# Optimization experiments

Measured on AMD Instinct MI355X. Metric: run time of the kernel, lower is better.

## Reference

```python
import jax, jax.numpy as jnp
import numpy as np

HEAD_SIZE = 64


def q_shift_multihead(x, ph, pw, head_dim=HEAD_SIZE, shift=1):
    # x: [B, T, C], T == ph*pw. Quarter-wise spatial shifts per head channel block.
    B, T, C = x.shape
    a = jnp.transpose(x, (0, 2, 1)).reshape(B, C // head_dim, head_dim, ph, pw)
    q = head_dim // 4
    out = jnp.zeros_like(a)
    out = out.at[:, :, 0:q, :, shift:].set(a[:, :, 0:q, :, :-shift])          # shift right in W
    out = out.at[:, :, q:2 * q, :, :-shift].set(a[:, :, q:2 * q, :, shift:])  # shift left in W
    out = out.at[:, :, 2 * q:3 * q, shift:, :].set(a[:, :, 2 * q:3 * q, :-shift, :])  # shift down in H
    out = out.at[:, :, 3 * q:, :-shift, :].set(a[:, :, 3 * q:, shift:, :])            # shift up in H
    return jnp.transpose(out.reshape(B, C, T), (0, 2, 1))


def wkv6(r, k, v, w, u):
    # RWKV-6 linear recurrence. r,k,v,w: [B,T,C]; u: [H, hs]. Decay applied as exp(-exp(w)).
    B, T, C = r.shape
    H, hs = C // HEAD_SIZE, HEAD_SIZE
    rh = jnp.transpose(r.reshape(B, T, H, hs), (1, 0, 2, 3))
    kh = jnp.transpose(k.reshape(B, T, H, hs), (1, 0, 2, 3))
    vh = jnp.transpose(v.reshape(B, T, H, hs), (1, 0, 2, 3))
    wh = jnp.exp(-jnp.exp(jnp.transpose(w.reshape(B, T, H, hs), (1, 0, 2, 3))))

    def step(S, inp):  # S: [B,H,hs(key j),hs(val i)]
        rt, kt, vt, wt = inp
        kv = kt[..., :, None] * vt[..., None, :]                # [B,H,hs,hs]
        y = jnp.einsum('bhj,bhji->bhi', rt, S + u[None, :, :, None] * kv)
        return wt[..., None] * S + kv, y

    S0 = jnp.zeros((B, H, hs, hs), r.dtype)
    _, ys = jax.lax.scan(step, S0, (rh, kh, vh, wh))
    return jnp.transpose(ys, (1, 0, 2, 3)).reshape(B, T, C)


def group_norm(x, weight, bias, n_groups, eps=1e-5):
    # x: [N, C]
    N, C = x.shape
    g = x.reshape(N, n_groups, C // n_groups)
    mu = g.mean(-1, keepdims=True)
    var = ((g - mu) ** 2).mean(-1, keepdims=True)
    g = (g - mu) / jnp.sqrt(var + eps)
    return g.reshape(N, C) * weight + bias


def setup_inputs() -> dict:
    key = jax.random.key(0)
    B, ph, pw, C = 8, 32, 32, 768
    T = ph * pw
    n_layer, layer_id = 12, 6
    H = C // HEAD_SIZE
    ks = jax.random.split(key, 10)
    x = jax.random.normal(ks[0], (B, T, C), jnp.float32)
    W_r = 0.02 * jax.random.normal(ks[1], (C, C), jnp.float32)
    W_k = 0.02 * jax.random.normal(ks[2], (C, C), jnp.float32)
    W_v = 0.02 * jax.random.normal(ks[3], (C, C), jnp.float32)
    W_g = 0.02 * jax.random.normal(ks[4], (C, C), jnp.float32)
    W_o = 0.02 * jax.random.normal(ks[5], (C, C), jnp.float32)
    r01 = layer_id / (n_layer - 1)
    r10 = 1.0 - layer_id / n_layer
    ddd = np.arange(C, dtype=np.float64) / C
    maa_x = jnp.asarray(1.0 - ddd ** r10, jnp.float32).reshape(1, 1, C)
    maa_w = maa_x
    maa_k = maa_x
    maa_v = jnp.asarray(1.0 - (ddd ** r10 + 0.3 * r01), jnp.float32).reshape(1, 1, C)
    maa_r = jnp.asarray(1.0 - ddd ** (0.5 * r10), jnp.float32).reshape(1, 1, C)
    maa_g = maa_r
    maa_w1 = jax.random.uniform(ks[6], (C, 32 * 5), jnp.float32, -1e-4, 1e-4)
    maa_w2 = jax.random.uniform(ks[7], (5, 32, C), jnp.float32, -1e-4, 1e-4)
    n = np.arange(C, dtype=np.float64)
    time_decay = jnp.asarray(-6 + 5 * (n / (C - 1)) ** (0.7 + 1.3 * r01), jnp.float32).reshape(1, 1, C)
    dec_w1 = jax.random.uniform(ks[8], (C, 64), jnp.float32, -1e-4, 1e-4)
    dec_w2 = jax.random.uniform(ks[9], (64, C), jnp.float32, -1e-4, 1e-4)
    zig = ((n + 1) % 3 - 1) * 0.1
    faaaa = jnp.asarray(r01 * (1 - n / (C - 1)) + zig, jnp.float32).reshape(H, HEAD_SIZE)
    ln_w = jnp.ones((C,), jnp.float32)
    ln_b = jnp.zeros((C,), jnp.float32)
    return dict(x=x, W_r=W_r, W_k=W_k, W_v=W_v, W_g=W_g, W_o=W_o,
                maa_x=maa_x, maa_w=maa_w, maa_k=maa_k, maa_v=maa_v, maa_r=maa_r, maa_g=maa_g,
                maa_w1=maa_w1, maa_w2=maa_w2, time_decay=time_decay,
                dec_w1=dec_w1, dec_w2=dec_w2, faaaa=faaaa, ln_w=ln_w, ln_b=ln_b,
                patch_h=ph, patch_w=pw)


def reference(x, W_r, W_k, W_v, W_g, W_o, maa_x, maa_w, maa_k, maa_v, maa_r, maa_g,
              maa_w1, maa_w2, time_decay, dec_w1, dec_w2, faaaa, ln_w, ln_b,
              patch_h, patch_w):
    B, T, C = x.shape
    xx = q_shift_multihead(x, patch_h, patch_w) - x
    xxx = x + xx * maa_x
    t = jnp.tanh(xxx @ maa_w1).reshape(B, T, 5, 32)
    m = jnp.einsum('btfr,frc->fbtc', t, maa_w2)  # [5,B,T,C]
    mw, mk, mv, mr, mg = m[0], m[1], m[2], m[3], m[4]
    xw = x + xx * (maa_w + mw)
    xk = x + xx * (maa_k + mk)
    xv = x + xx * (maa_v + mv)
    xr = x + xx * (maa_r + mr)
    xg = x + xx * (maa_g + mg)
    r = xr @ W_r.T
    k = xk @ W_k.T
    v = xv @ W_v.T
    g = jax.nn.relu(xg @ W_g.T)
    ww = jnp.tanh(xw @ dec_w1) @ dec_w2
    w = time_decay + ww
    y = wkv6(r, k, v, w, faaaa)
    y = group_norm(y.reshape(B * T, C), ln_w, ln_b, C // HEAD_SIZE).reshape(B, T, C)
    return (y * g) @ W_o.T
```

## Files before the change

### kernel.cpp

```cpp
#include <hip/hip_runtime.h>
#include <math.h>


#define EPI_NONE 0
#define EPI_TANH 1
#define EPI_RELU 2
#define EPI_BIAS 3

typedef float f32x4 __attribute__((ext_vector_type(4)));
typedef __bf16 bf16x8 __attribute__((ext_vector_type(8)));

__device__ __forceinline__ ushort f2bf(float x) {
  unsigned u = __float_as_uint(x);
  return (ushort)((u + 0x7fffu + ((u >> 16) & 1u)) >> 16);
}

#define GLDS16(gp, lp)                                                   \
  __builtin_amdgcn_global_load_lds(                                      \
      (const __attribute__((address_space(1))) void*)(gp),               \
      (__attribute__((address_space(3))) void*)(lp), 16, 0, 0)

__global__ __launch_bounds__(256) void k_qshift(
    const float* __restrict__ x, const float* __restrict__ maa_x,
    ushort* __restrict__ xxx_bf,
    int B, int T, int C, int ph, int pw) {
  long idx = (long)blockIdx.x * blockDim.x + threadIdx.x;
  long total = (long)B * T * C;
  if (idx >= total) return;
  int c = (int)(idx % C);
  long bt = idx / C;
  int t = (int)(bt % T);
  int quarter = (c & 63) >> 4;
  int hh = t / pw;
  int ww = t - hh * pw;
  long rowbase = (bt - t) * C;
  float sval = 0.f;
  int st = -1;
  if (quarter == 0)      { if (ww >= 1)      st = t - 1;  }
  else if (quarter == 1) { if (ww < pw - 1)  st = t + 1;  }
  else if (quarter == 2) { if (hh >= 1)      st = t - pw; }
  else                   { if (hh < ph - 1)  st = t + pw; }
  if (st >= 0) sval = x[rowbase + (long)st * C + c];
  float xval = x[idx];
  float d = sval - xval;
  xxx_bf[idx] = f2bf(xval + d * maa_x[c]);
}

__global__ __launch_bounds__(256) void k_wprep(
    const float* __restrict__ w1, const float* __restrict__ w2,
    const float* __restrict__ dw1, const float* __restrict__ dw2,
    ushort* __restrict__ maa1T, ushort* __restrict__ w2T,
    ushort* __restrict__ w1dT, ushort* __restrict__ w2dT) {
  int idx = blockIdx.x * 256 + threadIdx.x;
  if (idx < 196608) {
    int n = idx / 768, k = idx - n * 768;
    maa1T[idx] = f2bf(n < 160 ? w1[(size_t)k * 160 + n] : 0.f);
  } else if (idx < 196608 + 122880) {
    int j = idx - 196608;
    int c = j / 160, kk = j - c * 160;
    w2T[j] = f2bf(w2[(size_t)kk * 768 + c]);
  } else if (idx < 196608 + 122880 + 98304) {
    int j = idx - (196608 + 122880);
    int n = j / 768, k = j - n * 768;
    w1dT[j] = f2bf(n < 64 ? dw1[(size_t)k * 64 + n] : 0.f);
  } else {
    int j = idx - (196608 + 122880 + 98304);
    int n = j >> 6, k = j & 63;
    w2dT[j] = f2bf(dw2[(size_t)k * 768 + n]);
  }
}

__global__ __launch_bounds__(256) void k_mix5m(
    const ushort* __restrict__ t5b, const ushort* __restrict__ w2T,
    const float* __restrict__ x,
    const float* __restrict__ maa_w, const float* __restrict__ maa_k,
    const float* __restrict__ maa_v, const float* __restrict__ maa_r,
    const float* __restrict__ maa_g,
    ushort* __restrict__ xw, ushort* __restrict__ xk, ushort* __restrict__ xvb,
    ushort* __restrict__ xr, ushort* __restrict__ xg,
    int C, int T, int ph, int pw) {
  int tid = threadIdx.x;
  int lane = tid & 63, wid = tid >> 6;
  int m0 = blockIdx.y * 64, n0 = blockIdx.x * 128;
  int lm = lane & 15, lk = (lane >> 4) * 8;
  int rq = (lane >> 4) * 4;
  const ushort* ap = t5b + (size_t)(m0 + wid * 16 + lm) * 160 + lk;

  int stq[4][4];
#pragma unroll
  for (int q = 0; q < 4; q++) {
    int mr = m0 + wid * 16 + rq + q;
    int t = mr % T;
    int hh = t / pw, ww = t - hh * pw;
    stq[q][0] = (ww >= 1)      ? mr - 1  : -1;
    stq[q][1] = (ww < pw - 1)  ? mr + 1  : -1;
    stq[q][2] = (hh >= 1)      ? mr - pw : -1;
    stq[q][3] = (hh < ph - 1)  ? mr + pw : -1;
  }

  float xh[8][4], dh[8][4];
#pragma unroll
  for (int j = 0; j < 8; j++)
#pragma unroll
    for (int q = 0; q < 4; q++) {
      int mr = m0 + wid * 16 + rq + q;
      int col = n0 + j * 16 + lm;
      float xv = x[(size_t)mr * C + col];
      int sr = stq[q][j & 3];
      float sv = (sr >= 0) ? x[(size_t)sr * C + col] : 0.f;
      xh[j][q] = xv;
      dh[j][q] = sv - xv;
    }

#pragma unroll
  for (int f = 0; f < 5; f++) {
    bf16x8 af = *(const bf16x8*)(ap + f * 32);
    f32x4 acc[8];
#pragma unroll
    for (int j = 0; j < 8; j++) {
      bf16x8 bfj = *(const bf16x8*)(w2T +
          (size_t)(n0 + j * 16 + lm) * 160 + f * 32 + lk);
      acc[j] = __builtin_amdgcn_mfma_f32_16x16x32_bf16(
          af, bfj, (f32x4){0.f, 0.f, 0.f, 0.f}, 0, 0, 0);
    }
    const float* maa_f = (f == 0) ? maa_w : (f == 1) ? maa_k
                        : (f == 2) ? maa_v : (f == 3) ? maa_r : maa_g;
    ushort* dst = (f == 0) ? xw : (f == 1) ? xk
                 : (f == 2) ? xvb : (f == 3) ? xr : xg;
#pragma unroll
    for (int j = 0; j < 8; j++) {
      float mf = maa_f[n0 + j * 16 + lm];
#pragma unroll
      for (int q = 0; q < 4; q++) {
        size_t off = (size_t)(m0 + wid * 16 + rq + q) * C + (n0 + j * 16 + lm);
        dst[off] = f2bf(xh[j][q] + dh[j][q] * (mf + acc[j][q]));
      }
    }
  }
}

__global__ __launch_bounds__(256) void k_cvt5(
    const float* __restrict__ s0, const float* __restrict__ s1,
    const float* __restrict__ s2, const float* __restrict__ s3,
    const float* __restrict__ s4,
    ushort* __restrict__ d0, ushort* __restrict__ d1,
    ushort* __restrict__ d2, ushort* __restrict__ d3,
    ushort* __restrict__ d4, int n) {
  const float* s;
  ushort* d;
  switch (blockIdx.y) {
    case 0: s = s0; d = d0; break;
    case 1: s = s1; d = d1; break;
    case 2: s = s2; d = d2; break;
    case 3: s = s3; d = d3; break;
    default: s = s4; d = d4; break;
  }
  int i = (blockIdx.x * 256 + threadIdx.x) * 4;
  if (i >= n) return;
  float4 v = *(const float4*)(s + i);
  ushort4 o;
  o.x = f2bf(v.x); o.y = f2bf(v.y); o.z = f2bf(v.z); o.w = f2bf(v.w);
  *(ushort4*)(d + i) = o;
}

template <int EPI, bool NMASK, bool OBF16>
__global__ __launch_bounds__(256) void k_gemm_bf(
    const ushort* __restrict__ A, const ushort* __restrict__ W,
    const float* __restrict__ bias, void* __restrict__ Cm,
    int M, int N, int K) {
  __shared__ ushort Al[128 * 64];
  __shared__ ushort Bl[128 * 64];
  int nwg = gridDim.x * gridDim.y;
  int bid = blockIdx.y * gridDim.x + blockIdx.x;
  int swz = (nwg & 7) == 0 ? ((bid & 7) * (nwg >> 3) + (bid >> 3)) : bid;
  int bx = swz % gridDim.x, by = swz / gridDim.x;
  int m0 = by * 128, n0 = bx * 128;
  int tid = threadIdx.x;
  int lane = tid & 63, wave = tid >> 6;
  int wm = (wave >> 1) * 64, wn = (wave & 1) * 64;
  int lm = lane & 15, g = lane >> 4;
  f32x4 acc[4][4];
#pragma unroll
  for (int i = 0; i < 4; i++)
#pragma unroll
    for (int j = 0; j < 4; j++) acc[i][j] = (f32x4){0.f, 0.f, 0.f, 0.f};

  for (int k0 = 0; k0 < K; k0 += 64) {
#pragma unroll
    for (int i = 0; i < 4; i++) {
      int cid = tid + i * 256;
      int row = cid >> 3, p = cid & 7;
      int cq = p ^ (row & 7);
      GLDS16(A + (size_t)(m0 + row) * K + k0 + cq * 8, Al + cid * 8);
      GLDS16(W + (size_t)(n0 + row) * K + k0 + cq * 8, Bl + cid * 8);
    }
    __syncthreads();
#pragma unroll
    for (int s = 0; s < 2; s++) {
      bf16x8 af[4], bf[4];
#pragma unroll
      for (int i = 0; i < 4; i++) {
        int r = wm + i * 16 + lm;
        af[i] = *(const bf16x8*)&Al[r * 64 + (((s * 4 + g) ^ (r & 7)) * 8)];
        int rb = wn + i * 16 + lm;
        bf[i] = *(const bf16x8*)&Bl[rb * 64 + (((s * 4 + g) ^ (rb & 7)) * 8)];
      }
#pragma unroll
      for (int i = 0; i < 4; i++)
#pragma unroll
        for (int j = 0; j < 4; j++)
          acc[i][j] = __builtin_amdgcn_mfma_f32_16x16x32_bf16(
              af[i], bf[j], acc[i][j], 0, 0, 0);
    }
    __syncthreads();
  }
  int rq = (lane >> 4) * 4;
#pragma unroll
  for (int i = 0; i < 4; i++) {
#pragma unroll
    for (int j = 0; j < 4; j++) {
      int gn = n0 + wn + j * 16 + lm;
      if (NMASK && gn >= N) continue;
      float bv = (EPI == EPI_BIAS) ? bias[gn] : 0.f;
#pragma unroll
      for (int q = 0; q < 4; q++) {
        int gm = m0 + wm + i * 16 + rq + q;
        float val = acc[i][j][q];
        if (EPI == EPI_BIAS) val += bv;
        if (EPI == EPI_RELU) val = fmaxf(val, 0.f);
        if (EPI == EPI_TANH) val = tanhf(val);
        if (OBF16) ((ushort*)Cm)[(size_t)gm * N + gn] = f2bf(val);
        else       ((float*)Cm)[(size_t)gm * N + gn] = val;
      }
    }
  }
}

__global__ __launch_bounds__(256) void k_proj4(
    const ushort* __restrict__ A0, const ushort* __restrict__ A1,
    const ushort* __restrict__ A2, const ushort* __restrict__ A3,
    const ushort* __restrict__ W0, const ushort* __restrict__ W1,
    const ushort* __restrict__ W2, const ushort* __restrict__ W3,
    float* __restrict__ C0, float* __restrict__ C1,
    float* __restrict__ C2, float* __restrict__ C3,
    int M, int N, int K) {
  int nwg = gridDim.x;
  int bid = blockIdx.x;
  int swz = (bid & 7) * (nwg >> 3) + (bid >> 3);
  int nxt = N / 128;
  int per_z = (M / 128) * nxt;
  int z = swz / per_z;
  int rem = swz - z * per_z;
  int my = rem / nxt, nx = rem - my * nxt;
  const ushort* A = (z == 0) ? A0 : (z == 1) ? A1 : (z == 2) ? A2 : A3;
  const ushort* W = (z == 0) ? W0 : (z == 1) ? W1 : (z == 2) ? W2 : W3;
  float* Cm       = (z == 0) ? C0 : (z == 1) ? C1 : (z == 2) ? C2 : C3;
  __shared__ ushort Al[128 * 64];
  __shared__ ushort Bl[128 * 64];
  int tid = threadIdx.x;
  int m0 = my * 128, n0 = nx * 128;
  int lane = tid & 63, wave = tid >> 6;
  int wm = (wave >> 1) * 64, wn = (wave & 1) * 64;
  int lm = lane & 15, g = lane >> 4;
  f32x4 acc[4][4];
#pragma unroll
  for (int i = 0; i < 4; i++)
#pragma unroll
    for (int j = 0; j < 4; j++) acc[i][j] = (f32x4){0.f, 0.f, 0.f, 0.f};

  for (int k0 = 0; k0 < K; k0 += 64) {
#pragma unroll
    for (int i = 0; i < 4; i++) {
      int cid = tid + i * 256;
      int row = cid >> 3, p = cid & 7;
      int cq = p ^ (row & 7);
      GLDS16(A + (size_t)(m0 + row) * K + k0 + cq * 8, Al + cid * 8);
      GLDS16(W + (size_t)(n0 + row) * K + k0 + cq * 8, Bl + cid * 8);
    }
    __syncthreads();
#pragma unroll
    for (int s = 0; s < 2; s++) {
      bf16x8 af[4], bf[4];
#pragma unroll
      for (int i = 0; i < 4; i++) {
        int r = wm + i * 16 + lm;
        af[i] = *(const bf16x8*)&Al[r * 64 + (((s * 4 + g) ^ (r & 7)) * 8)];
        int rb = wn + i * 16 + lm;
        bf[i] = *(const bf16x8*)&Bl[rb * 64 + (((s * 4 + g) ^ (rb & 7)) * 8)];
      }
#pragma unroll
      for (int i = 0; i < 4; i++)
#pragma unroll
        for (int j = 0; j < 4; j++)
          acc[i][j] = __builtin_amdgcn_mfma_f32_16x16x32_bf16(
              af[i], bf[j], acc[i][j], 0, 0, 0);
    }
    __syncthreads();
  }
  bool relu = (z == 3);
  int rq = (lane >> 4) * 4;
#pragma unroll
  for (int i = 0; i < 4; i++) {
#pragma unroll
    for (int j = 0; j < 4; j++) {
      int gn = n0 + wn + j * 16 + lm;
#pragma unroll
      for (int q = 0; q < 4; q++) {
        int gm = m0 + wm + i * 16 + rq + q;
        float val = acc[i][j][q];
        if (relu) val = fmaxf(val, 0.f);
        Cm[(size_t)gm * N + gn] = val;
      }
    }
  }
}

__global__ __launch_bounds__(64) void k_wkv_pre(
    const float* __restrict__ r, const float* __restrict__ k,
    const float* __restrict__ w, const float* __restrict__ u,
    float* __restrict__ rt, float* __restrict__ kt,
    float* __restrict__ aL, float* __restrict__ pdiag,
    int B, int T, int C, int H, int L) {
  __shared__ float pls[64 * 65];
  int nch = T / L;
  int blk = blockIdx.x;
  int bh = blk / nch, c = blk - bh * nch;
  int b = bh / H, h = bh - b * H;
  int j = threadIdx.x;
  float uj = u[h * 64 + j];
  float cum = 0.f;
  long base = ((long)b * T + (long)c * L) * C + h * 64 + j;
  for (int tau = 0; tau < L; tau++) {
    long off = base + (long)tau * C;
    float wv = w[off];
    float rv = r[off];
    float kv = k[off];
    float e = expf(wv);
    rt[off] = rv * expf(-cum);
    cum += e;
    kt[off] = kv * expf(cum);
    pls[tau * 65 + j] = rv * uj * kv;
  }
  aL[((long)bh * nch + c) * 64 + j] = expf(-cum);
  __syncthreads();
  float s0 = 0.f, s1 = 0.f, s2 = 0.f, s3 = 0.f;
#pragma unroll
  for (int q = 0; q < 16; q++) {
    float4 p4 = *(const float4*)(pls + j * 65 + q * 4);
    s0 += p4.x; s1 += p4.y; s2 += p4.z; s3 += p4.w;
  }
  pdiag[(long)bh * T + c * L + j] = (s0 + s1) + (s2 + s3);
}

__global__ __launch_bounds__(256) void k_wkv_kv(
    const float* __restrict__ kt, const float* __restrict__ v,
    float* __restrict__ kvb, int B, int T, int C, int H, int L) {
  int nch = T / L;
  int blk = blockIdx.x;
  int bh = blk / nch, c = blk - bh * nch;
  int b = bh / H, h = bh - b * H;
  __shared__ float Ks[64 * 64];
  __shared__ float Vs[64 * 64];
  int tid = threadIdx.x;
  int lane = tid & 63, jg = tid >> 6;
  long cbase = ((long)b * T + (long)c * L) * C + h * 64;
#pragma unroll
  for (int i = 0; i < 4; i++) {
    int chunk = jg * 4 + i;
    int row = chunk * 4 + (lane >> 4);
    int cq = lane & 15;
    GLDS16(kt + cbase + (long)row * C + cq * 4, Ks + chunk * 256);
    GLDS16(v + cbase + (long)row * C + cq * 4, Vs + chunk * 256);
  }
  __syncthreads();
  float acc[16];
#pragma unroll
  for (int q = 0; q < 16; q++) acc[q] = 0.f;
  for (int s = 0; s < 64; s++) {
    float vi = Vs[s * 64 + lane];
#pragma unroll
    for (int q4 = 0; q4 < 4; q4++) {
      float4 kk = *(const float4*)(Ks + s * 64 + jg * 16 + q4 * 4);
      acc[q4 * 4 + 0] = fmaf(kk.x, vi, acc[q4 * 4 + 0]);
      acc[q4 * 4 + 1] = fmaf(kk.y, vi, acc[q4 * 4 + 1]);
      acc[q4 * 4 + 2] = fmaf(kk.z, vi, acc[q4 * 4 + 2]);
      acc[q4 * 4 + 3] = fmaf(kk.w, vi, acc[q4 * 4 + 3]);
    }
  }
  float* out = kvb + ((long)bh * nch + c) * 4096;
#pragma unroll
  for (int q = 0; q < 16; q++) out[(jg * 16 + q) * 64 + lane] = acc[q];
}

__global__ __launch_bounds__(256) void k_wkv_scan(
    const float* __restrict__ kvb, const float* __restrict__ aL,
    float* __restrict__ Scb, int nch) {
  int bh = blockIdx.x >> 4;
  int e = ((blockIdx.x & 15) << 8) + threadIdx.x;
  float S = 0.f;
  for (int c = 0; c < nch; c++) {
    long cb = ((long)bh * nch + c) * 4096 + e;
    Scb[cb] = S;
    S = aL[((long)bh * nch + c) * 64 + (e >> 6)] * (S + kvb[cb]);
  }
}

__global__ __launch_bounds__(256, 3) void k_wkv_intra(
    const float* __restrict__ rt, const float* __restrict__ kt,
    const float* __restrict__ v, const float* __restrict__ pdiag,
    const float* __restrict__ Scb, const float* __restrict__ g,
    const float* __restrict__ ln_w, const float* __restrict__ ln_b,
    ushort* __restrict__ z, int B, int T, int C, int H, int L) {
  int nch = T / L;
  int blk = blockIdx.x;
  int bh = blk / nch, c = blk - bh * nch;
  int b = bh / H, h = bh - b * H;
  __shared__ float KtT[64 * 68];
  __shared__ float RtT[64 * 68];
  __shared__ float Pt[64 * 68];
  int tid = threadIdx.x;
  int lane = tid & 63, wid = tid >> 6;
  long cbase = ((long)b * T + (long)c * L) * C + h * 64;
  const float* scp = Scb + ((long)bh * nch + c) * 4096;

  {
    int t0 = (tid >> 4) * 4;
    int c0s = (tid & 15) * 4;
    float4 ka[4], ra[4];
#pragma unroll
    for (int i = 0; i < 4; i++) {
      ka[i] = *(const float4*)(kt + cbase + (long)(t0 + i) * C + c0s);
      ra[i] = *(const float4*)(rt + cbase + (long)(t0 + i) * C + c0s);
    }
#pragma unroll
    for (int j = 0; j < 4; j++) {
      float4 ko, ro;
      ko.x = ka[0][j]; ko.y = ka[1][j]; ko.z = ka[2][j]; ko.w = ka[3][j];
      ro.x = ra[0][j]; ro.y = ra[1][j]; ro.z = ra[2][j]; ro.w = ra[3][j];
      *(float4*)(KtT + (c0s + j) * 68 + t0) = ko;
      *(float4*)(RtT + (c0s + j) * 68 + t0) = ro;
    }
  }
  __syncthreads();

  {
    int s0 = (tid >> 4) * 4;
    int tau0 = (tid & 15) * 4;
    float4 pd4 = *(const float4*)(pdiag + (long)bh * T + c * L + tau0);
    float p00 = 0.f, p01 = 0.f, p02 = 0.f, p03 = 0.f;
    float p10 = 0.f, p11 = 0.f, p12 = 0.f, p13 = 0.f;
    float p20 = 0.f, p21 = 0.f, p22 = 0.f, p23 = 0.f;
    float p30 = 0.f, p31 = 0.f, p32 = 0.f, p33 = 0.f;
#pragma unroll 4
    for (int cc = 0; cc < 64; cc++) {
      float4 kq = *(const float4*)(KtT + cc * 68 + s0);
      float4 rq = *(const float4*)(RtT + cc * 68 + tau0);
      p00 = fmaf(kq.x, rq.x, p00); p01 = fmaf(kq.x, rq.y, p01);
      p02 = fmaf(kq.x, rq.z, p02); p03 = fmaf(kq.x, rq.w, p03);
      p10 = fmaf(kq.y, rq.x, p10); p11 = fmaf(kq.y, rq.y, p11);
      p12 = fmaf(kq.y, rq.z, p12); p13 = fmaf(kq.y, rq.w, p13);
      p20 = fmaf(kq.z, rq.x, p20); p21 = fmaf(kq.z, rq.y, p21);
      p22 = fmaf(kq.z, rq.z, p22); p23 = fmaf(kq.z, rq.w, p23);
      p30 = fmaf(kq.w, rq.x, p30); p31 = fmaf(kq.w, rq.y, p31);
      p32 = fmaf(kq.w, rq.z, p32); p33 = fmaf(kq.w, rq.w, p33);
    }
#define PMASK(PI0, PI1, PI2, PI3, I)                                       \
    {                                                                      \
      int s = s0 + (I);                                                    \
      float4 o;                                                            \
      o.x = (s < tau0 + 0) ? PI0 : (s == tau0 + 0 ? pd4.x : 0.f);          \
      o.y = (s < tau0 + 1) ? PI1 : (s == tau0 + 1 ? pd4.y : 0.f);          \
      o.z = (s < tau0 + 2) ? PI2 : (s == tau0 + 2 ? pd4.z : 0.f);          \
      o.w = (s < tau0 + 3) ? PI3 : (s == tau0 + 3 ? pd4.w : 0.f);          \
      *(float4*)(Pt + s * 68 + tau0) = o;                                  \
    }
    PMASK(p00, p01, p02, p03, 0)
    PMASK(p10, p11, p12, p13, 1)
    PMASK(p20, p21, p22, p23, 2)
    PMASK(p30, p31, p32, p33, 3)
#undef PMASK
  }
  __syncthreads();

  int row0 = wid * 16 + ((lane >> 4) << 2);
  int c0v = (lane & 15) * 4;
  float4 acc0 = {0.f, 0.f, 0.f, 0.f};
  float4 acc1 = {0.f, 0.f, 0.f, 0.f};
  float4 acc2 = {0.f, 0.f, 0.f, 0.f};
  float4 acc3 = {0.f, 0.f, 0.f, 0.f};
  const float* vp = v + cbase + c0v;
#define FMA2(A, P, V4, R, S4)                          \
  A.x = fmaf(P, V4.x, fmaf(R, S4.x, A.x));             \
  A.y = fmaf(P, V4.y, fmaf(R, S4.y, A.y));             \
  A.z = fmaf(P, V4.z, fmaf(R, S4.z, A.z));             \
  A.w = fmaf(P, V4.w, fmaf(R, S4.w, A.w));
#pragma unroll 4
  for (int j = 0; j < 64; j++) {
    float4 pp = *(const float4*)(Pt + j * 68 + row0);
    float4 rr = *(const float4*)(RtT + j * 68 + row0);
    float4 vv = *(const float4*)(vp + (long)j * C);
    float4 ssv = *(const float4*)(scp + j * 64 + c0v);
    FMA2(acc0, pp.x, vv, rr.x, ssv);
    FMA2(acc1, pp.y, vv, rr.y, ssv);
    FMA2(acc2, pp.z, vv, rr.z, ssv);
    FMA2(acc3, pp.w, vv, rr.w, ssv);
  }
#undef FMA2

  float4 lw4 = *(const float4*)(ln_w + h * 64 + c0v);
  float4 lb4 = *(const float4*)(ln_b + h * 64 + c0v);
#define GNROW(A, m)                                                        \
  {                                                                        \
    float s1 = (A.x + A.y) + (A.z + A.w);                                  \
    s1 += __shfl_xor(s1, 1, 64);                                           \
    s1 += __shfl_xor(s1, 2, 64);                                           \
    s1 += __shfl_xor(s1, 4, 64);                                           \
    s1 += __shfl_xor(s1, 8, 64);                                           \
    float mu = s1 * (1.f / 64.f);                                          \
    float4 dd;                                                             \
    dd.x = A.x - mu; dd.y = A.y - mu; dd.z = A.z - mu; dd.w = A.w - mu;    \
    float s2 = (dd.x * dd.x + dd.y * dd.y) + (dd.z * dd.z + dd.w * dd.w);  \
    s2 += __shfl_xor(s2, 1, 64);                                           \
    s2 += __shfl_xor(s2, 2, 64);                                           \
    s2 += __shfl_xor(s2, 4, 64);                                           \
    s2 += __shfl_xor(s2, 8, 64);                                           \
    float rstd = rsqrtf(s2 * (1.f / 64.f) + 1e-5f);                        \
    long off = cbase + (long)(row0 + m) * C + c0v;                         \
    float4 g4 = *(const float4*)(g + off);                                 \
    ushort4 ob;                                                            \
    ob.x = f2bf((dd.x * rstd * lw4.x + lb4.x) * g4.x);                     \
    ob.y = f2bf((dd.y * rstd * lw4.y + lb4.y) * g4.y);                     \
    ob.z = f2bf((dd.z * rstd * lw4.z + lb4.z) * g4.z);                     \
    ob.w = f2bf((dd.w * rstd * lw4.w + lb4.w) * g4.w);                     \
    *(ushort4*)(z + off) = ob;                                             \
  }
  GNROW(acc0, 0)
  GNROW(acc1, 1)
  GNROW(acc2, 2)
  GNROW(acc3, 3)
#undef GNROW
}

extern "C" void kernel_launch(void* const* d_in, const int* in_sizes, int n_in,
                              void* d_out, int out_size, void* d_ws, size_t ws_size,
                              hipStream_t stream) {
  const int B = 8, T = 1024, C = 768, H = 12, ph = 32, pw = 32;
  const int M = B * T;
  const int L = 64, NCH = T / L;

  const float* x        = (const float*)d_in[0];
  const float* W_r      = (const float*)d_in[1];
  const float* W_k      = (const float*)d_in[2];
  const float* W_v      = (const float*)d_in[3];
  const float* W_g      = (const float*)d_in[4];
  const float* W_o      = (const float*)d_in[5];
  const float* maa_x    = (const float*)d_in[6];
  const float* maa_w    = (const float*)d_in[7];
  const float* maa_k    = (const float*)d_in[8];
  const float* maa_v    = (const float*)d_in[9];
  const float* maa_r    = (const float*)d_in[10];
  const float* maa_g    = (const float*)d_in[11];
  const float* maa_w1   = (const float*)d_in[12];
  const float* maa_w2   = (const float*)d_in[13];
  const float* time_dec = (const float*)d_in[14];
  const float* dec_w1   = (const float*)d_in[15];
  const float* dec_w2   = (const float*)d_in[16];
  const float* faaaa    = (const float*)d_in[17];
  const float* ln_w     = (const float*)d_in[18];
  const float* ln_b     = (const float*)d_in[19];

  float* ws = (float*)d_ws;
  const size_t S = (size_t)M * C;
  float* F0 = ws + 0 * S;
  float* F1 = ws + 1 * S;
  float* F2 = ws + 2 * S;
  float* F3 = ws + 3 * S;
  float* F4 = ws + 4 * S;
  float* F5 = ws + 5 * S;
  float* F6 = ws + 6 * S;
  float* t5    = ws + 7 * S;
  float* t6    = t5 + (size_t)M * 160;
  float* aLb   = t6 + (size_t)M * 64;
  float* pdiag = aLb + (size_t)B * H * NCH * 64;
  float* dec_t = pdiag + (size_t)B * H * T;

  ushort* xxx_bf = (ushort*)F1;
  ushort* xw_bf = (ushort*)F2;
  ushort* xr_bf = (ushort*)F5;
  ushort* xk_bf = xr_bf + S;
  ushort* xv_bf = (ushort*)F6;
  ushort* xg_bf = xv_bf + S;
  ushort* z_bf  = (ushort*)F6;
  ushort* t5b   = (ushort*)t5;
  ushort* t_bf  = (ushort*)dec_t;
  ushort* w2T   = t_bf + (size_t)M * 64;
  float* kvb = F0;
  float* Scb = F1;
  const int WSZ = C * C;
  ushort* wr_bf = (ushort*)t5;
  ushort* wk_bf = wr_bf + WSZ;
  ushort* wv_bf = wk_bf + WSZ;
  ushort* wg_bf = wv_bf + WSZ;
  ushort* wo_bf = (ushort*)t6;
  ushort* maa1T = wo_bf + WSZ;
  ushort* w1dT  = maa1T + 256 * 768;
  ushort* w2dT  = w1dT + 128 * 768;

  {
    long total = (long)M * C;
    k_qshift<<<(int)((total + 255) / 256), 256, 0, stream>>>(
        x, maa_x, xxx_bf, B, T, C, ph, pw);
  }
  {
    k_wprep<<<1824, 256, 0, stream>>>(maa_w1, maa_w2, dec_w1, dec_w2,
                                      maa1T, w2T, w1dT, w2dT);
    dim3 grid(2, M / 128);
    k_gemm_bf<EPI_TANH, true, true><<<grid, 256, 0, stream>>>(
        xxx_bf, maa1T, nullptr, t5b, M, 160, C);
  }
  {
    dim3 grid(C / 128, M / 64);
    k_mix5m<<<grid, 256, 0, stream>>>(t5b, w2T, x, maa_w, maa_k, maa_v,
                                      maa_r, maa_g, xw_bf, xk_bf, xv_bf, xr_bf,
                                      xg_bf, C, T, ph, pw);
  }
  {
    dim3 grid((WSZ / 4 + 255) / 256, 5);
    k_cvt5<<<grid, 256, 0, stream>>>(W_r, W_k, W_v, W_g, W_o,
                                     wr_bf, wk_bf, wv_bf, wg_bf, wo_bf, WSZ);
  }
  {
    k_proj4<<<(C / 128) * (M / 128) * 4, 256, 0, stream>>>(
        xr_bf, xk_bf, xv_bf, xg_bf, wr_bf, wk_bf, wv_bf, wg_bf,
        F0, F1, F3, F4, M, C, C);
  }
  {
    dim3 g1(1, M / 128);
    k_gemm_bf<EPI_TANH, true, true><<<g1, 256, 0, stream>>>(
        xw_bf, w1dT, nullptr, t_bf, M, 64, C);
    dim3 g2(C / 128, M / 128);
    k_gemm_bf<EPI_BIAS, false, false><<<g2, 256, 0, stream>>>(
        t_bf, w2dT, time_dec, F2, M, C, 64);
  }
  k_wkv_pre<<<B * H * NCH, 64, 0, stream>>>(F0, F1, F2, faaaa, F5, F2,
                                            aLb, pdiag, B, T, C, H, L);
  k_wkv_kv<<<B * H * NCH, 256, 0, stream>>>(F2, F3, kvb, B, T, C, H, L);
  k_wkv_scan<<<B * H * 16, 256, 0, stream>>>(kvb, aLb, Scb, NCH);
  k_wkv_intra<<<B * H * NCH, 256, 0, stream>>>(
      F5, F2, F3, pdiag, Scb, F4, ln_w, ln_b, z_bf, B, T, C, H, L);
  {
    dim3 grid(C / 128, M / 128);
    k_gemm_bf<EPI_NONE, false, false><<<grid, 256, 0, stream>>>(
        z_bf, wo_bf, nullptr, (float*)d_out, M, C, C);
  }
}
```

Measured before the change: 385.8 us.

## Fuse WKV preprocessing with chunk KV outer-product and merge prep kernels

```diff
diff --git a/kernel.cpp b/kernel.cpp
--- a/kernel.cpp
+++ b/kernel.cpp
@@ -20,38 +20,38 @@
       (const __attribute__((address_space(1))) void*)(gp),               \
       (__attribute__((address_space(3))) void*)(lp), 16, 0, 0)
 
-__global__ __launch_bounds__(256) void k_qshift(
+__global__ __launch_bounds__(256) void k_prep(
     const float* __restrict__ x, const float* __restrict__ maa_x,
     ushort* __restrict__ xxx_bf,
-    int B, int T, int C, int ph, int pw) {
-  long idx = (long)blockIdx.x * blockDim.x + threadIdx.x;
-  long total = (long)B * T * C;
-  if (idx >= total) return;
-  int c = (int)(idx % C);
-  long bt = idx / C;
-  int t = (int)(bt % T);
-  int quarter = (c & 63) >> 4;
-  int hh = t / pw;
-  int ww = t - hh * pw;
-  long rowbase = (bt - t) * C;
-  float sval = 0.f;
-  int st = -1;
-  if (quarter == 0)      { if (ww >= 1)      st = t - 1;  }
-  else if (quarter == 1) { if (ww < pw - 1)  st = t + 1;  }
-  else if (quarter == 2) { if (hh >= 1)      st = t - pw; }
-  else                   { if (hh < ph - 1)  st = t + pw; }
-  if (st >= 0) sval = x[rowbase + (long)st * C + c];
-  float xval = x[idx];
-  float d = sval - xval;
-  xxx_bf[idx] = f2bf(xval + d * maa_x[c]);
-}
-
-__global__ __launch_bounds__(256) void k_wprep(
     const float* __restrict__ w1, const float* __restrict__ w2,
     const float* __restrict__ dw1, const float* __restrict__ dw2,
     ushort* __restrict__ maa1T, ushort* __restrict__ w2T,
-    ushort* __restrict__ w1dT, ushort* __restrict__ w2dT) {
-  int idx = blockIdx.x * 256 + threadIdx.x;
+    ushort* __restrict__ w1dT, ushort* __restrict__ w2dT,
+    int B, int T, int C, int ph, int pw) {
+  long bx = blockIdx.x;
+  const long QBLK = 24576;
+  if (bx < QBLK) {
+    long idx = bx * 256 + threadIdx.x;
+    int c = (int)(idx % C);
+    long bt = idx / C;
+    int t = (int)(bt % T);
+    int quarter = (c & 63) >> 4;
+    int hh = t / pw;
+    int ww = t - hh * pw;
+    long rowbase = (bt - t) * C;
+    float sval = 0.f;
+    int st = -1;
+    if (quarter == 0)      { if (ww >= 1)      st = t - 1;  }
+    else if (quarter == 1) { if (ww < pw - 1)  st = t + 1;  }
+    else if (quarter == 2) { if (hh >= 1)      st = t - pw; }
+    else                   { if (hh < ph - 1)  st = t + pw; }
+    if (st >= 0) sval = x[rowbase + (long)st * C + c];
+    float xval = x[idx];
+    float d = sval - xval;
+    xxx_bf[idx] = f2bf(xval + d * maa_x[c]);
+    return;
+  }
+  int idx = (int)(bx - QBLK) * 256 + threadIdx.x;
   if (idx < 196608) {
     int n = idx / 768, k = idx - n * 768;
     maa1T[idx] = f2bf(n < 160 ? w1[(size_t)k * 160 + n] : 0.f);
@@ -315,64 +315,80 @@
   }
 }
 
-__global__ __launch_bounds__(64) void k_wkv_pre(
+__global__ __launch_bounds__(256) void k_wkv_prekv(
     const float* __restrict__ r, const float* __restrict__ k,
     const float* __restrict__ w, const float* __restrict__ u,
+    const float* __restrict__ v,
     float* __restrict__ rt, float* __restrict__ kt,
     float* __restrict__ aL, float* __restrict__ pdiag,
-    int B, int T, int C, int H, int L) {
-  __shared__ float pls[64 * 65];
+    float* __restrict__ kvb, int B, int T, int C, int H, int L) {
+  __shared__ float Ks[64 * 64];
+  __shared__ float Vs[64 * 64];
+  __shared__ float pls[64 * 68];
+  __shared__ float gsum[4 * 64];
   int nch = T / L;
   int blk = blockIdx.x;
   int bh = blk / nch, c = blk - bh * nch;
   int b = bh / H, h = bh - b * H;
-  int j = threadIdx.x;
+  int tid = threadIdx.x;
+  int gsel = tid >> 6;
+  int j = tid & 63;
+  long cbase = ((long)b * T + (long)c * L) * C + h * 64;
+
+#pragma unroll
+  for (int i = 0; i < 4; i++) {
+    int chunk = gsel * 4 + i;
+    int row = chunk * 4 + (j >> 4);
+    int cq = j & 15;
+    GLDS16(v + cbase + (long)row * C + cq * 4, Vs + chunk * 256);
+  }
+
+  int tau0 = gsel * 16;
   float uj = u[h * 64 + j];
-  float cum = 0.f;
-  long base = ((long)b * T + (long)c * L) * C + h * 64 + j;
-  for (int tau = 0; tau < L; tau++) {
-    long off = base + (long)tau * C;
-    float wv = w[off];
-    float rv = r[off];
-    float kv = k[off];
-    float e = expf(wv);
-    rt[off] = rv * expf(-cum);
-    cum += e;
-    kt[off] = kv * expf(cum);
-    pls[tau * 65 + j] = rv * uj * kv;
-  }
-  aL[((long)bh * nch + c) * 64 + j] = expf(-cum);
+  float ev[16];
+#pragma unroll
+  for (int i = 0; i < 16; i++)
+    ev[i] = expf(w[cbase + (long)(tau0 + i) * C + j]);
+  float pre[16];
+  float run = 0.f;
+#pragma unroll
+  for (int i = 0; i < 16; i++) { pre[i] = run; run += ev[i]; }
+  gsum[gsel * 64 + j] = run;
   __syncthreads();
-  float s0 = 0.f, s1 = 0.f, s2 = 0.f, s3 = 0.f;
-#pragma unroll
-  for (int q = 0; q < 16; q++) {
-    float4 p4 = *(const float4*)(pls + j * 65 + q * 4);
-    s0 += p4.x; s1 += p4.y; s2 += p4.z; s3 += p4.w;
-  }
-  pdiag[(long)bh * T + c * L + j] = (s0 + s1) + (s2 + s3);
-}
-
-__global__ __launch_bounds__(256) void k_wkv_kv(
-    const float* __restrict__ kt, const float* __restrict__ v,
-    float* __restrict__ kvb, int B, int T, int C, int H, int L) {
-  int nch = T / L;
-  int blk = blockIdx.x;
-  int bh = blk / nch, c = blk - bh * nch;
-  int b = bh / H, h = bh - b * H;
-  __shared__ float Ks[64 * 64];
-  __shared__ float Vs[64 * 64];
-  int tid = threadIdx.x;
+  float s0g = gsum[0 * 64 + j];
+  float s1g = gsum[1 * 64 + j];
+  float s2g = gsum[2 * 64 + j];
+  float off0 = (gsel > 0 ? s0g : 0.f) + (gsel > 1 ? s1g : 0.f) +
+               (gsel > 2 ? s2g : 0.f);
+  if (gsel == 3)
+    aL[((long)bh * nch + c) * 64 + j] = expf(-(off0 + run));
+
+#pragma unroll
+  for (int i = 0; i < 16; i++) {
+    long offg = cbase + (long)(tau0 + i) * C + j;
+    float rv = r[offg];
+    float kv = k[offg];
+    float ce = off0 + pre[i];
+    float rtv = rv * expf(-ce);
+    float ktv = kv * expf(ce + ev[i]);
+    rt[offg] = rtv;
+    kt[offg] = ktv;
+    Ks[(tau0 + i) * 64 + j] = ktv;
+    pls[(tau0 + i) * 68 + j] = rv * uj * kv;
+  }
+  __syncthreads();
+
+  if (tid < 64) {
+    float s0 = 0.f, s1 = 0.f, s2 = 0.f, s3 = 0.f;
+#pragma unroll
+    for (int q = 0; q < 16; q++) {
+      float4 p4 = *(const float4*)(pls + tid * 68 + q * 4);
+      s0 += p4.x; s1 += p4.y; s2 += p4.z; s3 += p4.w;
+    }
+    pdiag[(long)bh * T + c * L + tid] = (s0 + s1) + (s2 + s3);
+  }
+
   int lane = tid & 63, jg = tid >> 6;
-  long cbase = ((long)b * T + (long)c * L) * C + h * 64;
-#pragma unroll
-  for (int i = 0; i < 4; i++) {
-    int chunk = jg * 4 + i;
-    int row = chunk * 4 + (lane >> 4);
-    int cq = lane & 15;
-    GLDS16(kt + cbase + (long)row * C + cq * 4, Ks + chunk * 256);
-    GLDS16(v + cbase + (long)row * C + cq * 4, Vs + chunk * 256);
-  }
-  __syncthreads();
   float acc[16];
 #pragma unroll
   for (int q = 0; q < 16; q++) acc[q] = 0.f;
@@ -590,11 +606,11 @@
   ushort* xk_bf = xr_bf + S;
   ushort* xv_bf = (ushort*)F6;
   ushort* xg_bf = xv_bf + S;
+  float*  kvb   = F6;
   ushort* z_bf  = (ushort*)F6;
   ushort* t5b   = (ushort*)t5;
   ushort* t_bf  = (ushort*)dec_t;
   ushort* w2T   = t_bf + (size_t)M * 64;
-  float* kvb = F0;
   float* Scb = F1;
   const int WSZ = C * C;
   ushort* wr_bf = (ushort*)t5;
@@ -607,13 +623,11 @@
   ushort* w2dT  = w1dT + 128 * 768;
 
   {
-    long total = (long)M * C;
-    k_qshift<<<(int)((total + 255) / 256), 256, 0, stream>>>(
-        x, maa_x, xxx_bf, B, T, C, ph, pw);
-  }
-  {
-    k_wprep<<<1824, 256, 0, stream>>>(maa_w1, maa_w2, dec_w1, dec_w2,
-                                      maa1T, w2T, w1dT, w2dT);
+    k_prep<<<24576 + 1824, 256, 0, stream>>>(
+        x, maa_x, xxx_bf, maa_w1, maa_w2, dec_w1, dec_w2,
+        maa1T, w2T, w1dT, w2dT, B, T, C, ph, pw);
+  }
+  {
     dim3 grid(2, M / 128);
     k_gemm_bf<EPI_TANH, true, true><<<grid, 256, 0, stream>>>(
         xxx_bf, maa1T, nullptr, t5b, M, 160, C);
@@ -642,9 +656,8 @@
     k_gemm_bf<EPI_BIAS, false, false><<<g2, 256, 0, stream>>>(
         t_bf, w2dT, time_dec, F2, M, C, 64);
   }
-  k_wkv_pre<<<B * H * NCH, 64, 0, stream>>>(F0, F1, F2, faaaa, F5, F2,
-                                            aLb, pdiag, B, T, C, H, L);
-  k_wkv_kv<<<B * H * NCH, 256, 0, stream>>>(F2, F3, kvb, B, T, C, H, L);
+  k_wkv_prekv<<<B * H * NCH, 256, 0, stream>>>(
+      F0, F1, F2, faaaa, F3, F5, F2, aLb, pdiag, kvb, B, T, C, H, L);
   k_wkv_scan<<<B * H * 16, 256, 0, stream>>>(kvb, aLb, Scb, NCH);
   k_wkv_intra<<<B * H * NCH, 256, 0, stream>>>(
       F5, F2, F3, pdiag, Scb, F4, ln_w, ln_b, z_bf, B, T, C, H, L);
```

New measurement: 383.2 us. No clear change (-0.7%).
